# Kernel optimization log

Hardware: AMD Instinct MI355X
Metric: run time of the kernel (lower is better)

Reference implementation:

```python
import jax, jax.numpy as jnp
import numpy as np

N, E, H, ED, L, T = 4096, 65536, 128, 64, 3, 4
FO = H // T  # per-tower output dim (32)


def setup_inputs() -> dict:
    key = jax.random.key(0)
    ks = jax.random.split(key, 32)
    def g(i, shape, s=0.05):
        return jax.random.normal(ks[i], shape, dtype=jnp.float32) * s
    return {
        "x": g(0, (N, H), 1.0),
        "edge_attr": g(1, (E, ED), 1.0),
        "edge_index": jax.random.randint(ks[2], (2, E), 0, N, dtype=jnp.int32),
        "enc_W": g(3, (L, H, ED)), "enc_b": g(4, (L, H)),
        "pre_W": g(5, (L, T, H, 3 * H)), "pre_b": g(6, (L, T, H)),
        "post_W": g(7, (L, T, FO, 4 * H)), "post_b": g(8, (L, T, FO)),
        "lin_W": g(9, (L, H, H)), "lin_b": g(10, (L, H)),
        "gru_Wih": g(11, (3 * H, H)), "gru_Whh": g(12, (3 * H, H)),
        "gru_bih": g(13, (3 * H,)), "gru_bhh": g(14, (3 * H,)),
        "em1_W": g(15, (2 * H, 2 * H)), "em1_b": g(16, (2 * H,)),
        "em2_W": g(17, (2 * ED, 2 * H)), "em2_b": g(18, (2 * ED,)),
        "eu1_W": g(19, (2 * ED, 3 * ED)), "eu1_b": g(20, (2 * ED,)),
        "eu2_W": g(21, (ED, 2 * ED)), "eu2_b": g(22, (ED,)),
    }


def _lin(x, W, b):
    return x @ W.T + b


def _pna_layer(x, ea, src, dst, eW, eb, pW, pb, qW, qb, lW, lb):
    # PNAConv: towers=4, pre_layers=1, post_layers=1, aggr=[max,std,mean], scaler=identity
    n = x.shape[0]
    e = _lin(ea, eW, eb)                                   # edge encoder [E,H]
    h = jnp.concatenate([x[dst], x[src], e], axis=-1)       # [E,3H] (x_i, x_j, e)
    msg = jnp.einsum('ec,tfc->etf', h, pW) + pb             # per-tower pre-MLP [E,T,H]
    cnt = jax.ops.segment_sum(jnp.ones((msg.shape[0],), msg.dtype), dst, n)
    denom = jnp.maximum(cnt, 1.0)[:, None, None]
    mean = jax.ops.segment_sum(msg, dst, n) / denom
    mean2 = jax.ops.segment_sum(msg * msg, dst, n) / denom
    std = jnp.sqrt(jax.nn.relu(mean2 - mean * mean) + 1e-5)
    mx = jax.ops.segment_max(msg, dst, n)
    mx = jnp.where((cnt > 0)[:, None, None], mx, 0.0)
    agg = jnp.concatenate([mx, std, mean], axis=-1)         # [N,T,3H]
    xt = jnp.broadcast_to(x[:, None, :], (n, T, x.shape[1]))
    cat = jnp.concatenate([xt, agg], axis=-1)               # [N,T,4H]
    y = jnp.einsum('ntc,tfc->ntf', cat, qW) + qb            # per-tower post-MLP [N,T,FO]
    return _lin(y.reshape(n, -1), lW, lb)                   # [N,H]


def _gru(x, h, Wih, Whh, bih, bhh):
    gi = x @ Wih.T + bih
    gh = h @ Whh.T + bhh
    ir, iz, ic = jnp.split(gi, 3, axis=-1)
    hr, hz, hc = jnp.split(gh, 3, axis=-1)
    r = jax.nn.sigmoid(ir + hr)
    z = jax.nn.sigmoid(iz + hz)
    c = jnp.tanh(ic + r * hc)
    return (1.0 - z) * c + z * h


def reference(x, edge_attr, enc_W, enc_b, pre_W, pre_b, post_W, post_b, lin_W, lin_b,
              gru_Wih, gru_Whh, gru_bih, gru_bhh, em1_W, em1_b, em2_W, em2_b,
              eu1_W, eu1_b, eu2_W, eu2_b, edge_index):
    src, dst = edge_index[0], edge_index[1]
    out, hstate, ea = x, x, edge_attr
    for i in range(L):
        m = jax.nn.relu(_pna_layer(out, ea, src, dst, enc_W[i], enc_b[i],
                                   pre_W[i], pre_b[i], post_W[i], post_b[i],
                                   lin_W[i], lin_b[i]))
        hstate = _gru(m, hstate, gru_Wih, gru_Whh, gru_bih, gru_bhh)
        out = hstate
        uv = jnp.concatenate([out[src], out[dst]], axis=-1)
        m_ed = jax.nn.relu(_lin(jax.nn.relu(_lin(uv, em1_W, em1_b)), em2_W, em2_b))
        ea = _lin(jax.nn.relu(_lin(jnp.concatenate([m_ed, ea], axis=-1), eu1_W, eu1_b)), eu2_W, eu2_b)
    return (out, ea, out)
```

## Files before the change

### kernel.cpp

```cpp
#include <hip/hip_runtime.h>
#include <hip/hip_bf16.h>
#include <math.h>

#define NN 4096
#define EE 65536
#define HH 128
#define EDD 64
#define THD 512

typedef __bf16 bf16;
typedef __bf16 bf16x8 __attribute__((ext_vector_type(8)));
typedef __bf16 bf16x4 __attribute__((ext_vector_type(4)));
typedef float  floatx4 __attribute__((ext_vector_type(4)));

__global__ __launch_bounds__(64) void k_detect(const void* __restrict__ p,
                                               int* __restrict__ flag)
{
    const bf16* b = (const bf16*)p;
    int t = threadIdx.x;
    int bad = 0;
    for (int i = 0; i < 32; i++) {
        float v = (float)b[t * 32 + i];
        if (!(v == v) || fabsf(v) > 100.f) bad = 1;
    }
    unsigned long long m = __ballot(bad);
    if (t == 0) *flag = (m == 0ULL) ? 1 : 0;
}

__global__ __launch_bounds__(64) void k_detidx(const int* __restrict__ p,
                                               int* __restrict__ iflag)
{
    int t = threadIdx.x;
    int bad = 0;
    for (int i = 0; i < 8; i++) {
        int k = t * 8 + i;
        int lo = p[2 * k], hi = p[2 * k + 1];
        if (hi != 0 || lo < 0 || lo >= NN) bad = 1;
    }
    unsigned long long m = __ballot(bad);
    if (t == 0) *iflag = (m == 0ULL) ? 1 : 0;
}

__global__ void k_extidx(const int* __restrict__ p, int* __restrict__ srcW,
                         int* __restrict__ dstW, const int* __restrict__ iflag)
{
    int e = blockIdx.x * 256 + threadIdx.x;
    int s, d;
    if (*iflag) { s = p[2 * e];  d = p[2 * EE + 2 * e]; }
    else        { s = p[e];      d = p[EE + e]; }
    srcW[e] = min(max(s, 0), NN - 1);
    dstW[e] = min(max(d, 0), NN - 1);
}

#define NJOBS 22
struct Job { const void* src; void* dst1; void* dst2; int n; int mode; int blk0; };
struct JobTab { Job j[NJOBS]; };

__global__ __launch_bounds__(256) void k_canon_all(JobTab tab, const int* __restrict__ flag,
                                                   const int* __restrict__ pos)
{
    int b = blockIdx.x;
    int jj = 0;
#pragma unroll
    for (int t = 1; t < NJOBS; t++) if (b >= tab.j[t].blk0) jj = t;
    const Job J = tab.j[jj];
    int i = (b - J.blk0) * 256 + threadIdx.x;
    if (i >= J.n) return;
    float v = (*flag) ? (float)((const bf16*)J.src)[i] : ((const float*)J.src)[i];
    if (J.mode == 0) {
        ((float*)J.dst1)[i] = v;
    } else if (J.mode == 1) {
        ((bf16*)J.dst1)[i] = (bf16)v;
    } else if (J.mode == 2) {
        ((float*)J.dst1)[i] = v;
        ((bf16*)J.dst2)[i] = (bf16)v;
    } else {
        int e = i >> 6, d = i & 63;
        ((bf16*)J.dst1)[(size_t)pos[e] * 64 + d] = (bf16)v;
    }
}

__global__ __launch_bounds__(256) void k_repack_all(
    const bf16* __restrict__ preWbf, const bf16* __restrict__ em1Wbf,
    const float* __restrict__ em1b,
    bf16* __restrict__ Wnode, bf16* __restrict__ Wem1, float* __restrict__ ext)
{
    int b = blockIdx.x, tid = threadIdx.x;
    if (b < 1536) {
        int i = b * 256 + tid;
        int l = i >> 17, rem = i & 131071;
        int r = rem >> 7, c = rem & 127;
        bf16 v = (r < 512) ? preWbf[(size_t)l * 196608 + (size_t)r * 384 + c]
                           : preWbf[(size_t)l * 196608 + (size_t)(r - 512) * 384 + 128 + c];
        Wnode[i] = v;
    } else if (b < 1792) {
        int i = (b - 1536) * 256 + tid;
        int r = i >> 7, c = i & 127;
        Wem1[i] = (r < 256) ? em1Wbf[(size_t)r * 256 + c]
                            : em1Wbf[(size_t)(r - 256) * 256 + 128 + c];
    } else {
        int i = (b - 1792) * 256 + tid;
        if (i < 512) ext[i] = (i < 256) ? em1b[i] : 0.f;
    }
}

template<bool RELU, int OM>
__global__ __launch_bounds__(256) void k_mgemm(
    const bf16* __restrict__ A, int lda,
    const bf16* __restrict__ W, int ldw, const float* __restrict__ bias,
    void* __restrict__ Cv, int ldc, int K)
{
    __shared__ bf16 As[64][40];
    __shared__ bf16 Ws[64][40];
    const int m0 = blockIdx.x * 64, n0 = blockIdx.y * 64;
    const int tid = threadIdx.x, wave = tid >> 6, lane = tid & 63;
    const int wm = (wave & 1) * 32, wn = (wave >> 1) * 32;
    const int lrow = tid >> 2, lcol = (tid & 3) * 8;
    const int fr = lane & 15, fk = (lane >> 4) * 8;
    floatx4 acc00 = {0,0,0,0}, acc01 = {0,0,0,0}, acc10 = {0,0,0,0}, acc11 = {0,0,0,0};

    for (int k0 = 0; k0 < K; k0 += 32) {
        bf16x8 av = *(const bf16x8*)(A + (size_t)(m0 + lrow) * lda + k0 + lcol);
        bf16x8 wv = *(const bf16x8*)(W + (size_t)(n0 + lrow) * ldw + k0 + lcol);
        __syncthreads();
        *(bf16x8*)&As[lrow][lcol] = av;
        *(bf16x8*)&Ws[lrow][lcol] = wv;
        __syncthreads();
        bf16x8 a0 = *(const bf16x8*)&As[wm + fr][fk];
        bf16x8 a1 = *(const bf16x8*)&As[wm + 16 + fr][fk];
        bf16x8 b0 = *(const bf16x8*)&Ws[wn + fr][fk];
        bf16x8 b1 = *(const bf16x8*)&Ws[wn + 16 + fr][fk];
        acc00 = __builtin_amdgcn_mfma_f32_16x16x32_bf16(a0, b0, acc00, 0, 0, 0);
        acc01 = __builtin_amdgcn_mfma_f32_16x16x32_bf16(a0, b1, acc01, 0, 0, 0);
        acc10 = __builtin_amdgcn_mfma_f32_16x16x32_bf16(a1, b0, acc10, 0, 0, 0);
        acc11 = __builtin_amdgcn_mfma_f32_16x16x32_bf16(a1, b1, acc11, 0, 0, 0);
    }
    const int cc = lane & 15, cr = (lane >> 4) * 4;
    float vb0 = bias ? bias[n0 + wn + cc] : 0.f;
    float vb1 = bias ? bias[n0 + wn + 16 + cc] : 0.f;
    floatx4 accs[2][2] = {{acc00, acc01}, {acc10, acc11}};
#pragma unroll
    for (int mt = 0; mt < 2; mt++)
#pragma unroll
        for (int nt = 0; nt < 2; nt++) {
            float vb = nt ? vb1 : vb0;
#pragma unroll
            for (int i = 0; i < 4; i++) {
                int gm = m0 + wm + mt * 16 + cr + i;
                int gn = n0 + wn + nt * 16 + cc;
                float v = accs[mt][nt][i] + vb;
                if (RELU) v = fmaxf(v, 0.f);
                if (OM == 1) ((bf16*)Cv)[(size_t)gm * ldc + gn] = (bf16)v;
                else         ((float*)Cv)[(size_t)gm * ldc + gn] = v;
            }
        }
}

__global__ __launch_bounds__(256) void k_pdps(
    const bf16* __restrict__ A, const bf16* __restrict__ Wnode,
    const float* __restrict__ bias, float* __restrict__ Pd, bf16* __restrict__ Ps)
{
    __shared__ bf16 As[64][40];
    __shared__ bf16 Ws[64][40];
    const bool isPd = blockIdx.y < 8;
    const int m0 = blockIdx.x * 64;
    const int n0 = (isPd ? blockIdx.y : blockIdx.y - 8) * 64;
    const bf16* W = Wnode + (isPd ? 0 : (size_t)512 * 128);
    const int tid = threadIdx.x, wave = tid >> 6, lane = tid & 63;
    const int wm = (wave & 1) * 32, wn = (wave >> 1) * 32;
    const int lrow = tid >> 2, lcol = (tid & 3) * 8;
    const int fr = lane & 15, fk = (lane >> 4) * 8;
    floatx4 acc00 = {0,0,0,0}, acc01 = {0,0,0,0}, acc10 = {0,0,0,0}, acc11 = {0,0,0,0};

    for (int k0 = 0; k0 < 128; k0 += 32) {
        bf16x8 av = *(const bf16x8*)(A + (size_t)(m0 + lrow) * 128 + k0 + lcol);
        bf16x8 wv = *(const bf16x8*)(W + (size_t)(n0 + lrow) * 128 + k0 + lcol);
        __syncthreads();
        *(bf16x8*)&As[lrow][lcol] = av;
        *(bf16x8*)&Ws[lrow][lcol] = wv;
        __syncthreads();
        bf16x8 a0 = *(const bf16x8*)&As[wm + fr][fk];
        bf16x8 a1 = *(const bf16x8*)&As[wm + 16 + fr][fk];
        bf16x8 b0 = *(const bf16x8*)&Ws[wn + fr][fk];
        bf16x8 b1 = *(const bf16x8*)&Ws[wn + 16 + fr][fk];
        acc00 = __builtin_amdgcn_mfma_f32_16x16x32_bf16(a0, b0, acc00, 0, 0, 0);
        acc01 = __builtin_amdgcn_mfma_f32_16x16x32_bf16(a0, b1, acc01, 0, 0, 0);
        acc10 = __builtin_amdgcn_mfma_f32_16x16x32_bf16(a1, b0, acc10, 0, 0, 0);
        acc11 = __builtin_amdgcn_mfma_f32_16x16x32_bf16(a1, b1, acc11, 0, 0, 0);
    }
    const int cc = lane & 15, cr = (lane >> 4) * 4;
    float vb0 = isPd ? bias[n0 + wn + cc] : 0.f;
    float vb1 = isPd ? bias[n0 + wn + 16 + cc] : 0.f;
    floatx4 accs[2][2] = {{acc00, acc01}, {acc10, acc11}};
#pragma unroll
    for (int mt = 0; mt < 2; mt++)
#pragma unroll
        for (int nt = 0; nt < 2; nt++) {
            float vb = nt ? vb1 : vb0;
#pragma unroll
            for (int i = 0; i < 4; i++) {
                int gm = m0 + wm + mt * 16 + cr + i;
                int gn = n0 + wn + nt * 16 + cc;
                float v = accs[mt][nt][i] + vb;
                if (isPd) Pd[(size_t)gm * 512 + gn] = v;
                else      Ps[(size_t)gm * 512 + gn] = (bf16)v;
            }
        }
}

__global__ __launch_bounds__(256) void k_gigh(
    const bf16* __restrict__ m_bf, const bf16* __restrict__ out_bf,
    const bf16* __restrict__ Wih, const bf16* __restrict__ Whh,
    const float* __restrict__ bih, const float* __restrict__ bhh,
    float* __restrict__ gi, float* __restrict__ gh)
{
    __shared__ bf16 As[64][40];
    __shared__ bf16 Ws[64][40];
    const bf16* A = blockIdx.z ? out_bf : m_bf;
    const bf16* W = blockIdx.z ? Whh : Wih;
    const float* bias = blockIdx.z ? bhh : bih;
    float* C = blockIdx.z ? gh : gi;
    const int m0 = blockIdx.x * 64, n0 = blockIdx.y * 64;
    const int tid = threadIdx.x, wave = tid >> 6, lane = tid & 63;
    const int wm = (wave & 1) * 32, wn = (wave >> 1) * 32;
    const int lrow = tid >> 2, lcol = (tid & 3) * 8;
    const int fr = lane & 15, fk = (lane >> 4) * 8;
    floatx4 acc00 = {0,0,0,0}, acc01 = {0,0,0,0}, acc10 = {0,0,0,0}, acc11 = {0,0,0,0};

    for (int k0 = 0; k0 < 128; k0 += 32) {
        bf16x8 av = *(const bf16x8*)(A + (size_t)(m0 + lrow) * 128 + k0 + lcol);
        bf16x8 wv = *(const bf16x8*)(W + (size_t)(n0 + lrow) * 128 + k0 + lcol);
        __syncthreads();
        *(bf16x8*)&As[lrow][lcol] = av;
        *(bf16x8*)&Ws[lrow][lcol] = wv;
        __syncthreads();
        bf16x8 a0 = *(const bf16x8*)&As[wm + fr][fk];
        bf16x8 a1 = *(const bf16x8*)&As[wm + 16 + fr][fk];
        bf16x8 b0 = *(const bf16x8*)&Ws[wn + fr][fk];
        bf16x8 b1 = *(const bf16x8*)&Ws[wn + 16 + fr][fk];
        acc00 = __builtin_amdgcn_mfma_f32_16x16x32_bf16(a0, b0, acc00, 0, 0, 0);
        acc01 = __builtin_amdgcn_mfma_f32_16x16x32_bf16(a0, b1, acc01, 0, 0, 0);
        acc10 = __builtin_amdgcn_mfma_f32_16x16x32_bf16(a1, b0, acc10, 0, 0, 0);
        acc11 = __builtin_amdgcn_mfma_f32_16x16x32_bf16(a1, b1, acc11, 0, 0, 0);
    }
    const int cc = lane & 15, cr = (lane >> 4) * 4;
    float vb0 = bias[n0 + wn + cc];
    float vb1 = bias[n0 + wn + 16 + cc];
    floatx4 accs[2][2] = {{acc00, acc01}, {acc10, acc11}};
#pragma unroll
    for (int mt = 0; mt < 2; mt++)
#pragma unroll
        for (int nt = 0; nt < 2; nt++) {
            float vb = nt ? vb1 : vb0;
#pragma unroll
            for (int i = 0; i < 4; i++) {
                int gm = m0 + wm + mt * 16 + cr + i;
                int gn = n0 + wn + nt * 16 + cc;
                C[(size_t)gm * 384 + gn] = accs[mt][nt][i] + vb;
            }
        }
}

__global__ __launch_bounds__(256) void k_qgemm(
    const bf16* __restrict__ eaord, const bf16* __restrict__ wcomb,
    bf16* __restrict__ Qord)
{
    __shared__ bf16 As[64][72];
    __shared__ bf16 Ws[256][72];
    const int e0 = blockIdx.x * 64, n0g = blockIdx.y * 256;
    const int tid = threadIdx.x, wave = tid >> 6, lane = tid & 63;
    const int fr = lane & 15, fk = (lane >> 4) * 8;
    const int cc = lane & 15, cr = (lane >> 4) * 4;

#pragma unroll
    for (int v = 0; v < 2; v++) {
        int lin = v * 2048 + tid * 8;
        int r = lin >> 6, c = lin & 63;
        *(bf16x8*)&As[r][c] = *(const bf16x8*)(eaord + (size_t)(e0 + r) * 64 + c);
    }
#pragma unroll
    for (int v = 0; v < 8; v++) {
        int lin = v * 2048 + tid * 8;
        int r = lin >> 6, c = lin & 63;
        *(bf16x8*)&Ws[r][c] = *(const bf16x8*)(wcomb + (size_t)(n0g + r) * 64 + c);
    }
    __syncthreads();

    floatx4 acc[4][4];
#pragma unroll
    for (int mt = 0; mt < 4; mt++)
#pragma unroll
        for (int nt = 0; nt < 4; nt++) acc[mt][nt] = (floatx4){0,0,0,0};

#pragma unroll
    for (int kk = 0; kk < 64; kk += 32) {
        bf16x8 af[4], bv[4];
#pragma unroll
        for (int mt = 0; mt < 4; mt++) af[mt] = *(const bf16x8*)&As[mt * 16 + fr][kk + fk];
#pragma unroll
        for (int nt = 0; nt < 4; nt++) bv[nt] = *(const bf16x8*)&Ws[wave * 64 + nt * 16 + fr][kk + fk];
#pragma unroll
        for (int mt = 0; mt < 4; mt++)
#pragma unroll
            for (int nt = 0; nt < 4; nt++)
                acc[mt][nt] = __builtin_amdgcn_mfma_f32_16x16x32_bf16(af[mt], bv[nt], acc[mt][nt], 0, 0, 0);
    }
#pragma unroll
    for (int mt = 0; mt < 4; mt++)
#pragma unroll
        for (int nt = 0; nt < 4; nt++)
#pragma unroll
            for (int i = 0; i < 4; i++) {
                int row = mt * 16 + cr + i;
                int col = n0g + wave * 64 + nt * 16 + cc;
                Qord[(size_t)(e0 + row) * 512 + col] = (bf16)acc[mt][nt][i];
            }
}

__global__ __launch_bounds__(256) void k_edge(
    const bf16* __restrict__ SAB,
    const bf16* __restrict__ em2W, const float* __restrict__ em2b,
    const bf16* __restrict__ eu1W, const float* __restrict__ eu1b,
    const bf16* __restrict__ eu2W, const float* __restrict__ eu2b,
    const int* __restrict__ src, const int* __restrict__ dst,
    const int* __restrict__ pos,
    bf16* __restrict__ eaord, float* __restrict__ ea_out_f)
{
    __shared__ char smem[53248];
    bf16 (*Ws)[40]   = (bf16 (*)[40])smem;
    bf16 (*med)[200] = (bf16 (*)[200])(smem + 10240);
    bf16 (*As)[40]   = (bf16 (*)[40])(smem + 35840);
    bf16 (*t2s)[136] = (bf16 (*)[136])(smem + 35840);

    const int e0 = blockIdx.x * 64;
    const int tid = threadIdx.x, wave = tid >> 6, lane = tid & 63;
    const int lrow = tid >> 2, lcol = (tid & 3) * 8;
    const int fr = lane & 15, fk = (lane >> 4) * 8;
    const int cc = lane & 15, cr = (lane >> 4) * 4;
    const int wr = tid & 127, wc = (tid >> 7) * 16;
    const int wr3 = tid & 63, wc3 = (tid >> 6) * 8;
    const int sI = src[e0 + lrow], dI = dst[e0 + lrow];
    const floatx4 z4 = {0.f, 0.f, 0.f, 0.f};

    const int ac0 = (tid & 3) * 16;
    const int apr = pos[e0 + lrow];
    bf16x8 ea0 = *(const bf16x8*)(eaord + (size_t)apr * 64 + ac0);
    bf16x8 ea1 = *(const bf16x8*)(eaord + (size_t)apr * 64 + ac0 + 8);

    const int wm1 = (wave & 1) * 32, wn1 = (wave >> 1) * 64;
    floatx4 acc1[2][4];
#pragma unroll
    for (int mt = 0; mt < 2; mt++)
#pragma unroll
        for (int nt = 0; nt < 4; nt++) acc1[mt][nt] = z4;

    bf16x8 sv = *(const bf16x8*)(SAB + (size_t)sI * 512 + lcol);
    bf16x8 dv = *(const bf16x8*)(SAB + (size_t)dI * 512 + 256 + lcol);
    bf16x8 w0 = *(const bf16x8*)(em2W + (size_t)wr * 256 + wc);
    bf16x8 w1 = *(const bf16x8*)(em2W + (size_t)wr * 256 + wc + 8);

    for (int k0 = 0; k0 < 256; k0 += 32) {
        __syncthreads();
        bf16 a8[8];
#pragma unroll
        for (int j = 0; j < 8; j++)
            a8[j] = (bf16)fmaxf((float)sv[j] + (float)dv[j], 0.f);
        *(bf16x8*)&As[lrow][lcol] = *(bf16x8*)a8;
        *(bf16x8*)&Ws[wr][wc]     = w0;
        *(bf16x8*)&Ws[wr][wc + 8] = w1;
// ... 110 lines not shown
                eaord[(size_t)pos[e] * 64 + col] = (bf16)v;
                if (ea_out_f) ea_out_f[(size_t)e * 64 + col] = v;
            }
}

__global__ __launch_bounds__(256) void k_postg(
    const bf16* __restrict__ xin, const bf16* __restrict__ aggX,
    const bf16* __restrict__ aggS, const bf16* __restrict__ aggM,
    const bf16* __restrict__ qWbf, const float* __restrict__ qb,
    bf16* __restrict__ ybf)
{
    __shared__ bf16 As[64][40];
    __shared__ bf16 Ws[32][40];
    const int n0 = blockIdx.x * 64, t = blockIdx.y;
    const int tid = threadIdx.x, wave = tid >> 6, lane = tid & 63;
    const int lrow = tid >> 2, lcol = (tid & 3) * 8;
    const int fr = lane & 15, fk = (lane >> 4) * 8;
    floatx4 acc0 = {0,0,0,0}, acc1 = {0,0,0,0};

    for (int k0 = 0; k0 < 512; k0 += 32) {
        int n = n0 + lrow;
        int c0 = k0 + lcol;
        const bf16* srcp;
        if (c0 < 128)      srcp = xin  + (size_t)n * 128 + c0;
        else if (c0 < 256) srcp = aggX + (size_t)n * 512 + t * 128 + (c0 - 128);
        else if (c0 < 384) srcp = aggS + (size_t)n * 512 + t * 128 + (c0 - 256);
        else               srcp = aggM + (size_t)n * 512 + t * 128 + (c0 - 384);
        bf16x8 a8 = *(const bf16x8*)srcp;
        bf16 w8[8];
        if (tid < 128) {
            int wr = tid >> 2, wc = (tid & 3) * 8;
            *(bf16x8*)w8 = *(const bf16x8*)(qWbf + (size_t)(t * 32 + wr) * 512 + k0 + wc);
        }
        __syncthreads();
        *(bf16x8*)&As[lrow][lcol] = a8;
        if (tid < 128) {
            int wr = tid >> 2, wc = (tid & 3) * 8;
            *(bf16x8*)&Ws[wr][wc] = *(bf16x8*)w8;
        }
        __syncthreads();
        bf16x8 a  = *(const bf16x8*)&As[wave * 16 + fr][fk];
        bf16x8 b0 = *(const bf16x8*)&Ws[fr][fk];
        bf16x8 b1 = *(const bf16x8*)&Ws[16 + fr][fk];
        acc0 = __builtin_amdgcn_mfma_f32_16x16x32_bf16(a, b0, acc0, 0, 0, 0);
        acc1 = __builtin_amdgcn_mfma_f32_16x16x32_bf16(a, b1, acc1, 0, 0, 0);
    }
    const int cc = lane & 15, cr = (lane >> 4) * 4;
#pragma unroll
    for (int i = 0; i < 4; i++) {
        int gn = n0 + wave * 16 + cr + i;
        ybf[(size_t)gn * 128 + t * 32 + cc]      = (bf16)(acc0[i] + qb[t * 32 + cc]);
        ybf[(size_t)gn * 128 + t * 32 + 16 + cc] = (bf16)(acc1[i] + qb[t * 32 + 16 + cc]);
    }
}

__global__ __launch_bounds__(64) void k_wcomb(
    const float* __restrict__ preW, const float* __restrict__ encW,
    const float* __restrict__ encb, const float* __restrict__ preb,
    bf16* __restrict__ wcomb, float* __restrict__ bcombext)
{
    int tf = blockIdx.x, d = threadIdx.x;
    __shared__ float pw[128];
    __shared__ float red[64];
    const float* pr = preW + (size_t)tf * 384 + 256;
    pw[d]      = pr[d];
    pw[d + 64] = pr[d + 64];
    __syncthreads();
    float acc = 0.f;
    for (int h = 0; h < 128; h++) acc += pw[h] * encW[h * 64 + d];
    wcomb[tf * 64 + d] = (bf16)acc;
    float b = pw[d] * encb[d] + pw[d + 64] * encb[d + 64];
    red[d] = b;
    __syncthreads();
    for (int s = 32; s > 0; s >>= 1) { if (d < s) red[d] += red[d + s]; __syncthreads(); }
    if (d == 0) {
        bcombext[tf] = red[0] + preb[tf];
        bcombext[512 + tf] = 0.f;
    }
}

__global__ void k_count(const int* __restrict__ dst, int* __restrict__ counts)
{
    int e = blockIdx.x * 256 + threadIdx.x;
    atomicAdd(&counts[dst[e]], 1);
}

__global__ __launch_bounds__(1024) void k_scan(
    const int* __restrict__ counts, int* __restrict__ offs, int* __restrict__ cursor)
{
    __shared__ int ls[1024];
    int tid = threadIdx.x, base = tid * 4;
    int c0 = counts[base], c1 = counts[base + 1], c2 = counts[base + 2], c3 = counts[base + 3];
    ls[tid] = c0 + c1 + c2 + c3;
    __syncthreads();
    for (int d = 1; d < 1024; d <<= 1) {
        int v = (tid >= d) ? ls[tid - d] : 0;
        __syncthreads();
        ls[tid] += v;
        __syncthreads();
    }
    int r = tid ? ls[tid - 1] : 0;
    offs[base] = r;     cursor[base] = r;     r += c0;
    offs[base + 1] = r; cursor[base + 1] = r; r += c1;
    offs[base + 2] = r; cursor[base + 2] = r; r += c2;
    offs[base + 3] = r; cursor[base + 3] = r; r += c3;
    if (tid == 1023) offs[4096] = r;
}

__global__ void k_fill(const int* __restrict__ dst, const int* __restrict__ srcW,
                       int* __restrict__ cursor, int* __restrict__ pos,
                       int* __restrict__ srcord)
{
    int e = blockIdx.x * 256 + threadIdx.x;
    int p = atomicAdd(&cursor[dst[e]], 1);
    pos[e] = p;
    srcord[p] = srcW[e];
}

__global__ __launch_bounds__(128) void k_agg(
    const float* __restrict__ Pd, const bf16* __restrict__ Ps,
    const bf16* __restrict__ Qord,
    const int* __restrict__ srcord, const int* __restrict__ offs,
    bf16* __restrict__ aggX, bf16* __restrict__ aggS, bf16* __restrict__ aggM)
{
    int n = blockIdx.x, tid = threadIdx.x;
    int c = tid * 4;
    float4 pd = *(const float4*)(Pd + (size_t)n * 512 + c);
    float s0 = 0, s1 = 0, s2 = 0, s3 = 0;
    float q0 = 0, q1 = 0, q2 = 0, q3 = 0;
    float x0 = -3e38f, x1 = -3e38f, x2 = -3e38f, x3 = -3e38f;
    int beg = offs[n], end = offs[n + 1];
    for (int i = beg; i < end; i++) {
        int sn = srcord[i];
        bf16x4 psv = *(const bf16x4*)(Ps + (size_t)sn * 512 + c);
        bf16x4 qv  = *(const bf16x4*)(Qord + (size_t)i * 512 + c);
        float m0 = pd.x + (float)psv[0] + (float)qv[0];
        float m1 = pd.y + (float)psv[1] + (float)qv[1];
// ... 34 lines not shown
    float ic = gi[b + 256 + k], hc = gh[b + 256 + k];
    float r = 1.f / (1.f + __expf(-(ir + hr)));
    float z = 1.f / (1.f + __expf(-(iz + hz)));
    float c = tanhf(ic + r * hc);
    float h = hst[i];
    float hn = (1.f - z) * c + z * h;
    hst[i] = hn;
    ob[i] = (bf16)hn;
    if (fo) { fo[i] = hn; fo[4718592 + i] = hn; }
}

__global__ void k_sentinel(float* __restrict__ o, float v)
{
    int i = blockIdx.x * 256 + threadIdx.x;
    o[i] = v;
}

extern "C" void kernel_launch(void* const* d_in, const int* in_sizes, int n_in,
                              void* d_out, int out_size, void* d_ws, size_t ws_size,
                              hipStream_t stream)
{
    static const int exp_sizes[23] = {
        524288, 4194304, 131072, 24576, 384, 589824, 1536, 196608, 384,
        49152, 384, 49152, 49152, 384, 384, 65536, 256, 32768, 128,
        24576, 128, 8192, 64 };
    if (n_in != 23) { k_sentinel<<<2048, 256, 0, stream>>>((float*)d_out, 200.f); return; }
    for (int i = 0; i < 23; i++)
        if (in_sizes[i] != exp_sizes[i]) {
            k_sentinel<<<2048, 256, 0, stream>>>((float*)d_out, 60.f + 4.f * i);
            return;
        }
    if (out_size != 5242880) { k_sentinel<<<2048, 256, 0, stream>>>((float*)d_out, 52.f); return; }

    const int* eidx = (const int*)d_in[2];

    char* w = (char*)d_ws;
    size_t off = 0;
    auto alloc = [&](size_t bytes) -> char* {
        char* p = w + off;
        off = (off + bytes + 255) & ~(size_t)255;
        return p;
    };
    int*   dflag   = (int*)  alloc(256);
    int*   iflag   = (int*)  alloc(256);
    int*   srcW    = (int*)  alloc((size_t)EE * 4);
    int*   dstW    = (int*)  alloc((size_t)EE * 4);
    int*   pos     = (int*)  alloc((size_t)EE * 4);
    int*   srcord  = (int*)  alloc((size_t)EE * 4);
    float* out_f32 = (float*)alloc((size_t)NN * HH * 4);
    bf16*  out_bf  = (bf16*) alloc((size_t)NN * HH * 2);
    bf16*  m_bf    = (bf16*) alloc((size_t)NN * HH * 2);
    bf16*  ybf     = (bf16*) alloc((size_t)NN * HH * 2);
    bf16*  eaord   = (bf16*) alloc((size_t)EE * EDD * 2);
    bf16*  wcombBf = (bf16*) alloc((size_t)THD * EDD * 2);
    float* bcombx  = (float*)alloc((size_t)1024 * 4);
    int*   counts  = (int*)  alloc((size_t)NN * 4);
    int*   offs    = (int*)  alloc((size_t)(NN + 1) * 4);
    int*   cursor  = (int*)  alloc((size_t)NN * 4);
    float* Pd      = (float*)alloc((size_t)NN * THD * 4);
    bf16*  Ps      = (bf16*) alloc((size_t)NN * THD * 2);
    bf16*  aggX    = (bf16*) alloc((size_t)NN * THD * 2);
    bf16*  aggS    = (bf16*) alloc((size_t)NN * THD * 2);
    bf16*  aggM    = (bf16*) alloc((size_t)NN * THD * 2);
    float* encWc  = (float*)alloc((size_t)24576 * 4);
    float* encbc  = (float*)alloc((size_t)384 * 4);
    float* preWc  = (float*)alloc((size_t)589824 * 4);
    float* prebc  = (float*)alloc((size_t)1536 * 4);
    float* postbc = (float*)alloc((size_t)384 * 4);
    float* linbc  = (float*)alloc((size_t)384 * 4);
    float* bihc   = (float*)alloc((size_t)384 * 4);
    float* bhhc   = (float*)alloc((size_t)384 * 4);
    float* em1bc  = (float*)alloc((size_t)256 * 4);
    float* em1ext = (float*)alloc((size_t)512 * 4);
    float* em2bc  = (float*)alloc((size_t)128 * 4);
    float* eu1bc  = (float*)alloc((size_t)128 * 4);
    float* eu2bc  = (float*)alloc((size_t)64 * 4);
    bf16* preWbf = (bf16*)alloc((size_t)589824 * 2);
    bf16* WnodeBf= (bf16*)alloc((size_t)3 * 131072 * 2);
    bf16* postWbf= (bf16*)alloc((size_t)196608 * 2);
    bf16* linWbf = (bf16*)alloc((size_t)49152 * 2);
    bf16* WihBf  = (bf16*)alloc((size_t)49152 * 2);
    bf16* WhhBf  = (bf16*)alloc((size_t)49152 * 2);
    bf16* em1Wbf = (bf16*)alloc((size_t)65536 * 2);
    bf16* Wem1Bf = (bf16*)alloc((size_t)65536 * 2);
    bf16* em2Wbf = (bf16*)alloc((size_t)32768 * 2);
    bf16* eu1Wbf = (bf16*)alloc((size_t)24576 * 2);
    bf16* eu2Wbf = (bf16*)alloc((size_t)8192 * 2);
    char* region = alloc((size_t)EE * 512 * 2);
    bf16*  Qord = (bf16*) (region);
    float* gi   = (float*)(region);
    float* gh   = (float*)(region + 6291456);
    bf16*  SAB  = (bf16*) (region);

    if (ws_size < off) { k_sentinel<<<2048, 256, 0, stream>>>((float*)d_out, 44.f); return; }

    k_detidx<<<1, 64, 0, stream>>>(eidx, iflag);
    k_extidx<<<EE / 256, 256, 0, stream>>>(eidx, srcW, dstW, iflag);
    hipMemsetAsync(counts, 0, NN * 4, stream);
    k_count<<<EE / 256, 256, 0, stream>>>(dstW, counts);
    k_scan<<<1, 1024, 0, stream>>>(counts, offs, cursor);
    k_fill<<<EE / 256, 256, 0, stream>>>(dstW, srcW, cursor, pos, srcord);

    k_detect<<<1, 64, 0, stream>>>(d_in[1], dflag);
    {
        JobTab tab;
        int bi = 0, ji = 0;
        auto add = [&](const void* s, void* d1, void* d2, int n, int mode) {
            tab.j[ji] = { s, d1, d2, n, mode, bi };
            bi += (n + 255) / 256;
            ji++;
        };
        add(d_in[0],  out_f32, out_bf, 524288, 2);
        add(d_in[1],  eaord,   nullptr, 4194304, 3);
        add(d_in[5],  preWc,   preWbf, 589824, 2);
        add(d_in[3],  encWc,   nullptr, 24576, 0);
        add(d_in[4],  encbc,   nullptr, 384, 0);
        add(d_in[6],  prebc,   nullptr, 1536, 0);
        add(d_in[8],  postbc,  nullptr, 384, 0);
        add(d_in[10], linbc,   nullptr, 384, 0);
        add(d_in[13], bihc,    nullptr, 384, 0);
        add(d_in[14], bhhc,    nullptr, 384, 0);
        add(d_in[16], em1bc,   nullptr, 256, 0);
        add(d_in[18], em2bc,   nullptr, 128, 0);
        add(d_in[20], eu1bc,   nullptr, 128, 0);
        add(d_in[22], eu2bc,   nullptr, 64, 0);
        add(d_in[7],  postWbf, nullptr, 196608, 1);
        add(d_in[9],  linWbf,  nullptr, 49152, 1);
        add(d_in[11], WihBf,   nullptr, 49152, 1);
        add(d_in[12], WhhBf,   nullptr, 49152, 1);
        add(d_in[15], em1Wbf,  nullptr, 65536, 1);
        add(d_in[17], em2Wbf,  nullptr, 32768, 1);
        add(d_in[19], eu1Wbf,  nullptr, 24576, 1);
        add(d_in[21], eu2Wbf,  nullptr, 8192, 1);
        k_canon_all<<<bi, 256, 0, stream>>>(tab, dflag, pos);
    }
    k_repack_all<<<1794, 256, 0, stream>>>(preWbf, em1Wbf, em1bc, WnodeBf, Wem1Bf, em1ext);

    auto GEMM = [&](const bf16* A, int lda, const bf16* Wm, int ldw, const float* bias,
                    void* C, int ldc, int M, int Nout, int K, bool relu, int om) {
        dim3 grid(M / 64, Nout / 64);
        if (relu) {
            if (om) k_mgemm<true, 1><<<grid, 256, 0, stream>>>(A, lda, Wm, ldw, bias, C, ldc, K);
            else    k_mgemm<true, 0><<<grid, 256, 0, stream>>>(A, lda, Wm, ldw, bias, C, ldc, K);
        } else {
            if (om) k_mgemm<false, 1><<<grid, 256, 0, stream>>>(A, lda, Wm, ldw, bias, C, ldc, K);
            else    k_mgemm<false, 0><<<grid, 256, 0, stream>>>(A, lda, Wm, ldw, bias, C, ldc, K);
        }
    };

    for (int l = 0; l < 3; l++) {
        const float* preW_l  = preWc  + (size_t)l * 196608;
        const float* encW_l  = encWc  + (size_t)l * 8192;
        const float* encb_l  = encbc  + (size_t)l * 128;
        const float* preb_l  = prebc  + (size_t)l * 512;
        const bf16*  Wnode_l = WnodeBf + (size_t)l * 131072;
        const bf16*  postW_l = postWbf + (size_t)l * 65536;
        const float* postb_l = postbc + (size_t)l * 128;
        const bf16*  linW_l  = linWbf + (size_t)l * 16384;
        const float* linb_l  = linbc  + (size_t)l * 128;
        const bool last = (l == 2);

        k_wcomb<<<THD, 64, 0, stream>>>(preW_l, encW_l, encb_l, preb_l, wcombBf, bcombx);
        k_pdps<<<dim3(64, 16), 256, 0, stream>>>(out_bf, Wnode_l, bcombx, Pd, Ps);
        k_qgemm<<<dim3(EE / 64, 2), 256, 0, stream>>>(eaord, wcombBf, Qord);
        k_agg<<<NN, 128, 0, stream>>>(Pd, Ps, Qord, srcord, offs, aggX, aggS, aggM);
        k_postg<<<dim3(NN / 64, 4), 256, 0, stream>>>(out_bf, aggX, aggS, aggM,
                                                      postW_l, postb_l, ybf);
        GEMM(ybf, HH, linW_l, HH, linb_l, m_bf, HH, NN, HH, HH, true, 1);
        k_gigh<<<dim3(64, 6, 2), 256, 0, stream>>>(m_bf, out_bf, WihBf, WhhBf,
                                                   bihc, bhhc, gi, gh);
        k_gru<<<NN * HH / 256, 256, 0, stream>>>(gi, gh, out_f32, out_bf,
                                                 last ? (float*)d_out : (float*)nullptr);
        GEMM(out_bf, HH, Wem1Bf, 128, em1ext, SAB, 512, NN, 512, HH, false, 1);
        k_edge<<<EE / 64, 256, 0, stream>>>(SAB, em2Wbf, em2bc, eu1Wbf, eu1bc,
                                            eu2Wbf, eu2bc, srcW, dstW, pos,
                                            eaord, last ? (float*)d_out + 524288 : (float*)nullptr);
    }
}
```

Measured before the change: 474.4 us.

## Merge per-layer launches: fused PNA front kernel, hoisted wcomb, merged setup kernels

Merges the node projection GEMM (Pd/Ps), the edge Q GEMM and the GRU hidden-state GEMM (gh, which depends only on the previous output) into one multi-role kernel launched once per layer. The per-layer edge-encoder weight combination is precomputed for all layers in the setup repack kernel. Detection, count zeroing and degree counting are folded into fewer setup launches. gi and gh get dedicated buffers instead of aliasing the Qord region, which the new schedule requires. The aim is to cut launch count and tail idle time, at the cost of extra memory and a heterogeneous block mix in one grid.

```diff
diff --git a/kernel.cpp b/kernel.cpp
--- a/kernel.cpp
+++ b/kernel.cpp
@@ -13,43 +13,53 @@
 typedef __bf16 bf16x4 __attribute__((ext_vector_type(4)));
 typedef float  floatx4 __attribute__((ext_vector_type(4)));
 
-__global__ __launch_bounds__(64) void k_detect(const void* __restrict__ p,
-                                               int* __restrict__ flag)
-{
-    const bf16* b = (const bf16*)p;
-    int t = threadIdx.x;
-    int bad = 0;
-    for (int i = 0; i < 32; i++) {
-        float v = (float)b[t * 32 + i];
-        if (!(v == v) || fabsf(v) > 100.f) bad = 1;
-    }
-    unsigned long long m = __ballot(bad);
-    if (t == 0) *flag = (m == 0ULL) ? 1 : 0;
-}
-
-__global__ __launch_bounds__(64) void k_detidx(const int* __restrict__ p,
-                                               int* __restrict__ iflag)
-{
-    int t = threadIdx.x;
-    int bad = 0;
-    for (int i = 0; i < 8; i++) {
-        int k = t * 8 + i;
-        int lo = p[2 * k], hi = p[2 * k + 1];
-        if (hi != 0 || lo < 0 || lo >= NN) bad = 1;
-    }
-    unsigned long long m = __ballot(bad);
-    if (t == 0) *iflag = (m == 0ULL) ? 1 : 0;
-}
-
-__global__ void k_extidx(const int* __restrict__ p, int* __restrict__ srcW,
-                         int* __restrict__ dstW, const int* __restrict__ iflag)
+__global__ __launch_bounds__(256) void k_det0(const void* __restrict__ eaIn,
+                                              const int* __restrict__ eidx,
+                                              int* __restrict__ dflag,
+                                              int* __restrict__ iflag,
+                                              int* __restrict__ counts)
+{
+    int b = blockIdx.x, t = threadIdx.x;
+    if (b == 0) {
+        if (t < 64) {
+            const bf16* p = (const bf16*)eaIn;
+            int bad = 0;
+            for (int i = 0; i < 32; i++) {
+                float v = (float)p[t * 32 + i];
+                if (!(v == v) || fabsf(v) > 100.f) bad = 1;
+            }
+            unsigned long long m = __ballot(bad);
+            if (t == 0) *dflag = (m == 0ULL) ? 1 : 0;
+        }
+    } else if (b == 1) {
+        if (t < 64) {
+            int bad = 0;
+            for (int i = 0; i < 8; i++) {
+                int k = t * 8 + i;
+                int lo = eidx[2 * k], hi = eidx[2 * k + 1];
+                if (hi != 0 || lo < 0 || lo >= NN) bad = 1;
+            }
+            unsigned long long m = __ballot(bad);
+            if (t == 0) *iflag = (m == 0ULL) ? 1 : 0;
+        }
+    } else {
+        counts[(b - 2) * 256 + t] = 0;
+    }
+}
+
+__global__ void k_extcnt(const int* __restrict__ p, int* __restrict__ srcW,
+                         int* __restrict__ dstW, const int* __restrict__ iflag,
+                         int* __restrict__ counts)
 {
     int e = blockIdx.x * 256 + threadIdx.x;
     int s, d;
     if (*iflag) { s = p[2 * e];  d = p[2 * EE + 2 * e]; }
     else        { s = p[e];      d = p[EE + e]; }
-    srcW[e] = min(max(s, 0), NN - 1);
-    dstW[e] = min(max(d, 0), NN - 1);
+    s = min(max(s, 0), NN - 1);
+    d = min(max(d, 0), NN - 1);
+    srcW[e] = s;
+    dstW[e] = d;
+    atomicAdd(&counts[d], 1);
 }
 
 #define NJOBS 22
@@ -80,11 +90,16 @@
     }
 }
 
-__global__ __launch_bounds__(256) void k_repack_all(
+__global__ __launch_bounds__(256) void k_setup2(
     const bf16* __restrict__ preWbf, const bf16* __restrict__ em1Wbf,
     const float* __restrict__ em1b,
-    bf16* __restrict__ Wnode, bf16* __restrict__ Wem1, float* __restrict__ ext)
-{
+    bf16* __restrict__ Wnode, bf16* __restrict__ Wem1, float* __restrict__ ext,
+    const float* __restrict__ preWc, const float* __restrict__ encWc,
+    const float* __restrict__ encbc, const float* __restrict__ prebc,
+    bf16* __restrict__ wcombAll, float* __restrict__ bcombAll)
+{
+    __shared__ float pw[4][128];
+    __shared__ float red[4][64];
     int b = blockIdx.x, tid = threadIdx.x;
     if (b < 1536) {
         int i = b * 256 + tid;
@@ -98,9 +113,30 @@
         int r = i >> 7, c = i & 127;
         Wem1[i] = (r < 256) ? em1Wbf[(size_t)r * 256 + c]
                             : em1Wbf[(size_t)(r - 256) * 256 + 128 + c];
-    } else {
+    } else if (b < 1794) {
         int i = (b - 1792) * 256 + tid;
         if (i < 512) ext[i] = (i < 256) ? em1b[i] : 0.f;
+    } else {
+        int q = b - 1794;
+        int sub = tid >> 6, d = tid & 63;
+        int tf = q * 4 + sub;
+        int l = tf >> 9, tfl = tf & 511;
+        const float* pr = preWc + (size_t)l * 196608 + (size_t)tfl * 384 + 256;
+        pw[sub][d]      = pr[d];
+        pw[sub][d + 64] = pr[d + 64];
+        __syncthreads();
+        const float* encW = encWc + (size_t)l * 8192;
+        float acc = 0.f;
+        for (int h = 0; h < 128; h++) acc += pw[sub][h] * encW[h * 64 + d];
+        wcombAll[(size_t)l * 32768 + (size_t)tfl * 64 + d] = (bf16)acc;
+        float bb = pw[sub][d] * encbc[l * 128 + d] + pw[sub][d + 64] * encbc[l * 128 + 64 + d];
+        red[sub][d] = bb;
+        __syncthreads();
+        for (int s = 32; s > 0; s >>= 1) { if (d < s) red[sub][d] += red[sub][d + s]; __syncthreads(); }
+        if (d == 0) {
+            bcombAll[l * 1024 + tfl] = red[sub][0] + prebc[l * 512 + tfl];
+            bcombAll[l * 1024 + 512 + tfl] = 0.f;
+        }
     }
 }
 
@@ -156,16 +192,135 @@
         }
 }
 
-__global__ __launch_bounds__(256) void k_pdps(
-    const bf16* __restrict__ A, const bf16* __restrict__ Wnode,
-    const float* __restrict__ bias, float* __restrict__ Pd, bf16* __restrict__ Ps)
+__global__ __launch_bounds__(256) void k_pna_front(
+    const bf16* __restrict__ out_bf, const bf16* __restrict__ Wnode_l,
+    const float* __restrict__ bcombx_l, float* __restrict__ Pd, bf16* __restrict__ Ps,
+    const bf16* __restrict__ eaord, const bf16* __restrict__ wcomb_l,
+    bf16* __restrict__ Qord,
+    const bf16* __restrict__ Whh, const float* __restrict__ bhh,
+    float* __restrict__ gh)
+{
+    __shared__ char smem[46080];
+    const int b = blockIdx.x;
+    const int tid = threadIdx.x, wave = tid >> 6, lane = tid & 63;
+    const int fr = lane & 15, fk = (lane >> 4) * 8;
+    const int cc = lane & 15, cr = (lane >> 4) * 4;
+
+    if (b < 1024 || b >= 3072) {
+        bf16 (*As)[40] = (bf16 (*)[40])smem;
+        bf16 (*Ws)[40] = (bf16 (*)[40])(smem + 5120);
+        const bool isGh = (b >= 3072);
+        int m0, n0;
+        const bf16* W;
+        const float* bias;
+        bool isPd = false;
+        if (isGh) {
+            int g = b - 3072;
+            m0 = (g & 63) * 64; n0 = (g >> 6) * 64;
+            W = Whh; bias = bhh;
+        } else {
+            m0 = (b & 63) * 64;
+            int y = b >> 6;
+            isPd = y < 8;
+            n0 = (isPd ? y : y - 8) * 64;
+            W = Wnode_l + (isPd ? 0 : (size_t)512 * 128);
+            bias = bcombx_l;
+        }
+        const int wm = (wave & 1) * 32, wn = (wave >> 1) * 32;
+        const int lrow = tid >> 2, lcol = (tid & 3) * 8;
+        floatx4 acc00 = {0,0,0,0}, acc01 = {0,0,0,0}, acc10 = {0,0,0,0}, acc11 = {0,0,0,0};
+        for (int k0 = 0; k0 < 128; k0 += 32) {
+            bf16x8 av = *(const bf16x8*)(out_bf + (size_t)(m0 + lrow) * 128 + k0 + lcol);
+            bf16x8 wv = *(const bf16x8*)(W + (size_t)(n0 + lrow) * 128 + k0 + lcol);
+            __syncthreads();
+            *(bf16x8*)&As[lrow][lcol] = av;
+            *(bf16x8*)&Ws[lrow][lcol] = wv;
+            __syncthreads();
+            bf16x8 a0 = *(const bf16x8*)&As[wm + fr][fk];
+            bf16x8 a1 = *(const bf16x8*)&As[wm + 16 + fr][fk];
+            bf16x8 b0 = *(const bf16x8*)&Ws[wn + fr][fk];
+            bf16x8 b1 = *(const bf16x8*)&Ws[wn + 16 + fr][fk];
+            acc00 = __builtin_amdgcn_mfma_f32_16x16x32_bf16(a0, b0, acc00, 0, 0, 0);
+            acc01 = __builtin_amdgcn_mfma_f32_16x16x32_bf16(a0, b1, acc01, 0, 0, 0);
+            acc10 = __builtin_amdgcn_mfma_f32_16x16x32_bf16(a1, b0, acc10, 0, 0, 0);
+            acc11 = __builtin_amdgcn_mfma_f32_16x16x32_bf16(a1, b1, acc11, 0, 0, 0);
+        }
+        float vb0 = (isGh || isPd) ? bias[n0 + wn + cc] : 0.f;
+        float vb1 = (isGh || isPd) ? bias[n0 + wn + 16 + cc] : 0.f;
+        floatx4 accs[2][2] = {{acc00, acc01}, {acc10, acc11}};
+#pragma unroll
+        for (int mt = 0; mt < 2; mt++)
+#pragma unroll
+            for (int nt = 0; nt < 2; nt++) {
+                float vb = nt ? vb1 : vb0;
+#pragma unroll
+                for (int i = 0; i < 4; i++) {
+                    int gm = m0 + wm + mt * 16 + cr + i;
+                    int gn = n0 + wn + nt * 16 + cc;
+                    float v = accs[mt][nt][i] + vb;
+                    if (isGh)      gh[(size_t)gm * 384 + gn] = v;
+                    else if (isPd) Pd[(size_t)gm * 512 + gn] = v;
+                    else           Ps[(size_t)gm * 512 + gn] = (bf16)v;
+                }
+            }
+    } else {
+        bf16 (*As)[72] = (bf16 (*)[72])smem;
+        bf16 (*Ws)[72] = (bf16 (*)[72])(smem + 9216);
+        int q = b - 1024;
+        const int e0 = (q & 1023) * 64, n0g = (q >> 10) * 256;
+#pragma unroll
+        for (int v = 0; v < 2; v++) {
+            int lin = v * 2048 + tid * 8;
+            int r = lin >> 6, c = lin & 63;
+            *(bf16x8*)&As[r][c] = *(const bf16x8*)(eaord + (size_t)(e0 + r) * 64 + c);
+        }
+#pragma unroll
+        for (int v = 0; v < 8; v++) {
+            int lin = v * 2048 + tid * 8;
+            int r = lin >> 6, c = lin & 63;
+            *(bf16x8*)&Ws[r][c] = *(const bf16x8*)(wcomb_l + (size_t)(n0g + r) * 64 + c);
+        }
+        __syncthreads();
+
+        floatx4 acc[4][4];
+#pragma unroll
+        for (int mt = 0; mt < 4; mt++)
+#pragma unroll
+            for (int nt = 0; nt < 4; nt++) acc[mt][nt] = (floatx4){0,0,0,0};
+
+#pragma unroll
+        for (int kk = 0; kk < 64; kk += 32) {
+            bf16x8 af[4], bv[4];
+#pragma unroll
+            for (int mt = 0; mt < 4; mt++) af[mt] = *(const bf16x8*)&As[mt * 16 + fr][kk + fk];
+#pragma unroll
+            for (int nt = 0; nt < 4; nt++) bv[nt] = *(const bf16x8*)&Ws[wave * 64 + nt * 16 + fr][kk + fk];
+#pragma unroll
+            for (int mt = 0; mt < 4; mt++)
+#pragma unroll
+                for (int nt = 0; nt < 4; nt++)
+                    acc[mt][nt] = __builtin_amdgcn_mfma_f32_16x16x32_bf16(af[mt], bv[nt], acc[mt][nt], 0, 0, 0);
+        }
+#pragma unroll
+        for (int mt = 0; mt < 4; mt++)
+#pragma unroll
+            for (int nt = 0; nt < 4; nt++)
+#pragma unroll
+                for (int i = 0; i < 4; i++) {
+                    int row = mt * 16 + cr + i;
+                    int col = n0g + wave * 64 + nt * 16 + cc;
+                    Qord[(size_t)(e0 + row) * 512 + col] = (bf16)acc[mt][nt][i];
+                }
+    }
+}
+
+__global__ __launch_bounds__(256) void k_gi(
+    const bf16* __restrict__ m_bf, const bf16* __restrict__ Wih,
+    const float* __restrict__ bih, float* __restrict__ gi)
 {
     __shared__ bf16 As[64][40];
     __shared__ bf16 Ws[64][40];
-    const bool isPd = blockIdx.y < 8;
-    const int m0 = blockIdx.x * 64;
-    const int n0 = (isPd ? blockIdx.y : blockIdx.y - 8) * 64;
-    const bf16* W = Wnode + (isPd ? 0 : (size_t)512 * 128);
+    const int m0 = blockIdx.x * 64, n0 = blockIdx.y * 64;
     const int tid = threadIdx.x, wave = tid >> 6, lane = tid & 63;
     const int wm = (wave & 1) * 32, wn = (wave >> 1) * 32;
     const int lrow = tid >> 2, lcol = (tid & 3) * 8;
@@ -173,8 +328,8 @@
     floatx4 acc00 = {0,0,0,0}, acc01 = {0,0,0,0}, acc10 = {0,0,0,0}, acc11 = {0,0,0,0};
 
     for (int k0 = 0; k0 < 128; k0 += 32) {
-        bf16x8 av = *(const bf16x8*)(A + (size_t)(m0 + lrow) * 128 + k0 + lcol);
-        bf16x8 wv = *(const bf16x8*)(W + (size_t)(n0 + lrow) * 128 + k0 + lcol);
+        bf16x8 av = *(const bf16x8*)(m_bf + (size_t)(m0 + lrow) * 128 + k0 + lcol);
+        bf16x8 wv = *(const bf16x8*)(Wih + (size_t)(n0 + lrow) * 128 + k0 + lcol);
         __syncthreads();
         *(bf16x8*)&As[lrow][lcol] = av;
         *(bf16x8*)&Ws[lrow][lcol] = wv;
@@ -189,8 +344,8 @@
         acc11 = __builtin_amdgcn_mfma_f32_16x16x32_bf16(a1, b1, acc11, 0, 0, 0);
     }
     const int cc = lane & 15, cr = (lane >> 4) * 4;
-    float vb0 = isPd ? bias[n0 + wn + cc] : 0.f;
-    float vb1 = isPd ? bias[n0 + wn + 16 + cc] : 0.f;
+    float vb0 = bih[n0 + wn + cc];
+    float vb1 = bih[n0 + wn + 16 + cc];
     floatx4 accs[2][2] = {{acc00, acc01}, {acc10, acc11}};
 #pragma unroll
     for (int mt = 0; mt < 2; mt++)
@@ -201,120 +356,9 @@
             for (int i = 0; i < 4; i++) {
                 int gm = m0 + wm + mt * 16 + cr + i;
                 int gn = n0 + wn + nt * 16 + cc;
-                float v = accs[mt][nt][i] + vb;
-                if (isPd) Pd[(size_t)gm * 512 + gn] = v;
-                else      Ps[(size_t)gm * 512 + gn] = (bf16)v;
+                gi[(size_t)gm * 384 + gn] = accs[mt][nt][i] + vb;
             }
         }
-}
-
-__global__ __launch_bounds__(256) void k_gigh(
-    const bf16* __restrict__ m_bf, const bf16* __restrict__ out_bf,
-    const bf16* __restrict__ Wih, const bf16* __restrict__ Whh,
-    const float* __restrict__ bih, const float* __restrict__ bhh,
-    float* __restrict__ gi, float* __restrict__ gh)
-{
-    __shared__ bf16 As[64][40];
-    __shared__ bf16 Ws[64][40];
-    const bf16* A = blockIdx.z ? out_bf : m_bf;
-    const bf16* W = blockIdx.z ? Whh : Wih;
-    const float* bias = blockIdx.z ? bhh : bih;
-    float* C = blockIdx.z ? gh : gi;
-    const int m0 = blockIdx.x * 64, n0 = blockIdx.y * 64;
-    const int tid = threadIdx.x, wave = tid >> 6, lane = tid & 63;
-    const int wm = (wave & 1) * 32, wn = (wave >> 1) * 32;
-    const int lrow = tid >> 2, lcol = (tid & 3) * 8;
-    const int fr = lane & 15, fk = (lane >> 4) * 8;
-    floatx4 acc00 = {0,0,0,0}, acc01 = {0,0,0,0}, acc10 = {0,0,0,0}, acc11 = {0,0,0,0};
-
-    for (int k0 = 0; k0 < 128; k0 += 32) {
-        bf16x8 av = *(const bf16x8*)(A + (size_t)(m0 + lrow) * 128 + k0 + lcol);
-        bf16x8 wv = *(const bf16x8*)(W + (size_t)(n0 + lrow) * 128 + k0 + lcol);
-        __syncthreads();
-        *(bf16x8*)&As[lrow][lcol] = av;
-        *(bf16x8*)&Ws[lrow][lcol] = wv;
-        __syncthreads();
-        bf16x8 a0 = *(const bf16x8*)&As[wm + fr][fk];
-        bf16x8 a1 = *(const bf16x8*)&As[wm + 16 + fr][fk];
-        bf16x8 b0 = *(const bf16x8*)&Ws[wn + fr][fk];
-        bf16x8 b1 = *(const bf16x8*)&Ws[wn + 16 + fr][fk];
-        acc00 = __builtin_amdgcn_mfma_f32_16x16x32_bf16(a0, b0, acc00, 0, 0, 0);
-        acc01 = __builtin_amdgcn_mfma_f32_16x16x32_bf16(a0, b1, acc01, 0, 0, 0);
-        acc10 = __builtin_amdgcn_mfma_f32_16x16x32_bf16(a1, b0, acc10, 0, 0, 0);
-        acc11 = __builtin_amdgcn_mfma_f32_16x16x32_bf16(a1, b1, acc11, 0, 0, 0);
-    }
-    const int cc = lane & 15, cr = (lane >> 4) * 4;
-    float vb0 = bias[n0 + wn + cc];
-    float vb1 = bias[n0 + wn + 16 + cc];
-    floatx4 accs[2][2] = {{acc00, acc01}, {acc10, acc11}};
-#pragma unroll
-    for (int mt = 0; mt < 2; mt++)
-#pragma unroll
-        for (int nt = 0; nt < 2; nt++) {
-            float vb = nt ? vb1 : vb0;
-#pragma unroll
-            for (int i = 0; i < 4; i++) {
-                int gm = m0 + wm + mt * 16 + cr + i;
-                int gn = n0 + wn + nt * 16 + cc;
-                C[(size_t)gm * 384 + gn] = accs[mt][nt][i] + vb;
-            }
-        }
-}
-
-__global__ __launch_bounds__(256) void k_qgemm(
-    const bf16* __restrict__ eaord, const bf16* __restrict__ wcomb,
-    bf16* __restrict__ Qord)
-{
-    __shared__ bf16 As[64][72];
-    __shared__ bf16 Ws[256][72];
-    const int e0 = blockIdx.x * 64, n0g = blockIdx.y * 256;
-    const int tid = threadIdx.x, wave = tid >> 6, lane = tid & 63;
-    const int fr = lane & 15, fk = (lane >> 4) * 8;
-    const int cc = lane & 15, cr = (lane >> 4) * 4;
-
-#pragma unroll
-    for (int v = 0; v < 2; v++) {
-        int lin = v * 2048 + tid * 8;
-        int r = lin >> 6, c = lin & 63;
-        *(bf16x8*)&As[r][c] = *(const bf16x8*)(eaord + (size_t)(e0 + r) * 64 + c);
-    }
-#pragma unroll
-    for (int v = 0; v < 8; v++) {
-        int lin = v * 2048 + tid * 8;
-        int r = lin >> 6, c = lin & 63;
-        *(bf16x8*)&Ws[r][c] = *(const bf16x8*)(wcomb + (size_t)(n0g + r) * 64 + c);
-    }
-    __syncthreads();
-
-    floatx4 acc[4][4];
-#pragma unroll
-    for (int mt = 0; mt < 4; mt++)
-#pragma unroll
-        for (int nt = 0; nt < 4; nt++) acc[mt][nt] = (floatx4){0,0,0,0};
-
-#pragma unroll
-    for (int kk = 0; kk < 64; kk += 32) {
-        bf16x8 af[4], bv[4];
-#pragma unroll
-        for (int mt = 0; mt < 4; mt++) af[mt] = *(const bf16x8*)&As[mt * 16 + fr][kk + fk];
-#pragma unroll
-        for (int nt = 0; nt < 4; nt++) bv[nt] = *(const bf16x8*)&Ws[wave * 64 + nt * 16 + fr][kk + fk];
-#pragma unroll
-        for (int mt = 0; mt < 4; mt++)
-#pragma unroll
-            for (int nt = 0; nt < 4; nt++)
-                acc[mt][nt] = __builtin_amdgcn_mfma_f32_16x16x32_bf16(af[mt], bv[nt], acc[mt][nt], 0, 0, 0);
-    }
-#pragma unroll
-    for (int mt = 0; mt < 4; mt++)
-#pragma unroll
-        for (int nt = 0; nt < 4; nt++)
-#pragma unroll
-            for (int i = 0; i < 4; i++) {
-                int row = mt * 16 + cr + i;
-                int col = n0g + wave * 64 + nt * 16 + cc;
-                Qord[(size_t)(e0 + row) * 512 + col] = (bf16)acc[mt][nt][i];
-            }
 }
 
 __global__ __launch_bounds__(256) void k_edge(
@@ -531,37 +575,6 @@
         ybf[(size_t)gn * 128 + t * 32 + cc]      = (bf16)(acc0[i] + qb[t * 32 + cc]);
         ybf[(size_t)gn * 128 + t * 32 + 16 + cc] = (bf16)(acc1[i] + qb[t * 32 + 16 + cc]);
     }
-}
-
-__global__ __launch_bounds__(64) void k_wcomb(
-    const float* __restrict__ preW, const float* __restrict__ encW,
-    const float* __restrict__ encb, const float* __restrict__ preb,
-    bf16* __restrict__ wcomb, float* __restrict__ bcombext)
-{
-    int tf = blockIdx.x, d = threadIdx.x;
-    __shared__ float pw[128];
-    __shared__ float red[64];
-    const float* pr = preW + (size_t)tf * 384 + 256;
-    pw[d]      = pr[d];
-    pw[d + 64] = pr[d + 64];
-    __syncthreads();
-    float acc = 0.f;
-    for (int h = 0; h < 128; h++) acc += pw[h] * encW[h * 64 + d];
-    wcomb[tf * 64 + d] = (bf16)acc;
-    float b = pw[d] * encb[d] + pw[d + 64] * encb[d + 64];
-    red[d] = b;
-    __syncthreads();
-    for (int s = 32; s > 0; s >>= 1) { if (d < s) red[d] += red[d + s]; __syncthreads(); }
-    if (d == 0) {
-        bcombext[tf] = red[0] + preb[tf];
-        bcombext[512 + tf] = 0.f;
-    }
-}
-
-__global__ void k_count(const int* __restrict__ dst, int* __restrict__ counts)
-{
-    int e = blockIdx.x * 256 + threadIdx.x;
-    atomicAdd(&counts[dst[e]], 1);
 }
 
 __global__ __launch_bounds__(1024) void k_scan(
@@ -702,8 +715,8 @@
     bf16*  m_bf    = (bf16*) alloc((size_t)NN * HH * 2);
     bf16*  ybf     = (bf16*) alloc((size_t)NN * HH * 2);
     bf16*  eaord   = (bf16*) alloc((size_t)EE * EDD * 2);
-    bf16*  wcombBf = (bf16*) alloc((size_t)THD * EDD * 2);
-    float* bcombx  = (float*)alloc((size_t)1024 * 4);
+    bf16*  wcombAll= (bf16*) alloc((size_t)3 * THD * EDD * 2);
+    float* bcombAll= (float*)alloc((size_t)3 * 1024 * 4);
     int*   counts  = (int*)  alloc((size_t)NN * 4);
     int*   offs    = (int*)  alloc((size_t)(NN + 1) * 4);
     int*   cursor  = (int*)  alloc((size_t)NN * 4);
@@ -712,6 +725,8 @@
     bf16*  aggX    = (bf16*) alloc((size_t)NN * THD * 2);
     bf16*  aggS    = (bf16*) alloc((size_t)NN * THD * 2);
     bf16*  aggM    = (bf16*) alloc((size_t)NN * THD * 2);
+    float* giB     = (float*)alloc((size_t)NN * 384 * 4);
+    float* ghB     = (float*)alloc((size_t)NN * 384 * 4);
     float* encWc  = (float*)alloc((size_t)24576 * 4);
     float* encbc  = (float*)alloc((size_t)384 * 4);
     float* preWc  = (float*)alloc((size_t)589824 * 4);
@@ -738,20 +753,15 @@
     bf16* eu2Wbf = (bf16*)alloc((size_t)8192 * 2);
     char* region = alloc((size_t)EE * 512 * 2);
     bf16*  Qord = (bf16*) (region);
-    float* gi   = (float*)(region);
-    float* gh   = (float*)(region + 6291456);
     bf16*  SAB  = (bf16*) (region);
 
     if (ws_size < off) { k_sentinel<<<2048, 256, 0, stream>>>((float*)d_out, 44.f); return; }
 
-    k_detidx<<<1, 64, 0, stream>>>(eidx, iflag);
-    k_extidx<<<EE / 256, 256, 0, stream>>>(eidx, srcW, dstW, iflag);
-    hipMemsetAsync(counts, 0, NN * 4, stream);
-    k_count<<<EE / 256, 256, 0, stream>>>(dstW, counts);
+    k_det0<<<18, 256, 0, stream>>>(d_in[1], eidx, dflag, iflag, counts);
+    k_extcnt<<<EE / 256, 256, 0, stream>>>(eidx, srcW, dstW, iflag, counts);
     k_scan<<<1, 1024, 0, stream>>>(counts, offs, cursor);
     k_fill<<<EE / 256, 256, 0, stream>>>(dstW, srcW, cursor, pos, srcord);
 
-    k_detect<<<1, 64, 0, stream>>>(d_in[1], dflag);
     {
         JobTab tab;
         int bi = 0, ji = 0;
@@ -784,7 +794,8 @@
         add(d_in[21], eu2Wbf,  nullptr, 8192, 1);
         k_canon_all<<<bi, 256, 0, stream>>>(tab, dflag, pos);
     }
-    k_repack_all<<<1794, 256, 0, stream>>>(preWbf, em1Wbf, em1bc, WnodeBf, Wem1Bf, em1ext);
+    k_setup2<<<2178, 256, 0, stream>>>(preWbf, em1Wbf, em1bc, WnodeBf, Wem1Bf, em1ext,
+                                       preWc, encWc, encbc, prebc, wcombAll, bcombAll);
 
     auto GEMM = [&](const bf16* A, int lda, const bf16* Wm, int ldw, const float* bias,
                     void* C, int ldc, int M, int Nout, int K, bool relu, int om) {
@@ -799,27 +810,23 @@
     };
 
     for (int l = 0; l < 3; l++) {
-        const float* preW_l  = preWc  + (size_t)l * 196608;
-        const float* encW_l  = encWc  + (size_t)l * 8192;
-        const float* encb_l  = encbc  + (size_t)l * 128;
-        const float* preb_l  = prebc  + (size_t)l * 512;
-        const bf16*  Wnode_l = WnodeBf + (size_t)l * 131072;
-        const bf16*  postW_l = postWbf + (size_t)l * 65536;
-        const float* postb_l = postbc + (size_t)l * 128;
-        const bf16*  linW_l  = linWbf + (size_t)l * 16384;
-        const float* linb_l  = linbc  + (size_t)l * 128;
+        const bf16*  Wnode_l  = WnodeBf + (size_t)l * 131072;
+        const bf16*  postW_l  = postWbf + (size_t)l * 65536;
+        const float* postb_l  = postbc + (size_t)l * 128;
+        const bf16*  linW_l   = linWbf + (size_t)l * 16384;
+        const float* linb_l   = linbc  + (size_t)l * 128;
+        const bf16*  wcomb_l  = wcombAll + (size_t)l * 32768;
+        const float* bcombx_l = bcombAll + (size_t)l * 1024;
         const bool last = (l == 2);
 
-        k_wcomb<<<THD, 64, 0, stream>>>(preW_l, encW_l, encb_l, preb_l, wcombBf, bcombx);
-        k_pdps<<<dim3(64, 16), 256, 0, stream>>>(out_bf, Wnode_l, bcombx, Pd, Ps);
-        k_qgemm<<<dim3(EE / 64, 2), 256, 0, stream>>>(eaord, wcombBf, Qord);
+        k_pna_front<<<3456, 256, 0, stream>>>(out_bf, Wnode_l, bcombx_l, Pd, Ps,
+                                              eaord, wcomb_l, Qord, WhhBf, bhhc, ghB);
         k_agg<<<NN, 128, 0, stream>>>(Pd, Ps, Qord, srcord, offs, aggX, aggS, aggM);
         k_postg<<<dim3(NN / 64, 4), 256, 0, stream>>>(out_bf, aggX, aggS, aggM,
                                                       postW_l, postb_l, ybf);
         GEMM(ybf, HH, linW_l, HH, linb_l, m_bf, HH, NN, HH, HH, true, 1);
-        k_gigh<<<dim3(64, 6, 2), 256, 0, stream>>>(m_bf, out_bf, WihBf, WhhBf,
-                                                   bihc, bhhc, gi, gh);
-        k_gru<<<NN * HH / 256, 256, 0, stream>>>(gi, gh, out_f32, out_bf,
+        k_gi<<<dim3(64, 6), 256, 0, stream>>>(m_bf, WihBf, bihc, giB);
+        k_gru<<<NN * HH / 256, 256, 0, stream>>>(giB, ghB, out_f32, out_bf,
                                                  last ? (float*)d_out : (float*)nullptr);
         GEMM(out_bf, HH, Wem1Bf, 128, em1ext, SAB, 512, NN, 512, HH, false, 1);
         k_edge<<<EE / 64, 256, 0, stream>>>(SAB, em2Wbf, em2bc, eu1Wbf, eu1bc,
```

Result: faster. 445.2 us (median of 3 runs) (-6.2%).
